# Optimization experiments

Hardware: AMD Instinct MI355X
Metric: run time of the kernel (lower is better)

The kernel has to match this reference:

```python
import jax, jax.numpy as jnp
import numpy as np

D = 256
H = 4
DH = D // H
DFF = 1024
EPS = 1e-5


def _split_heads(x):
    B, L, _ = x.shape
    return x.reshape(B, L, H, DH).transpose(0, 2, 1, 3)  # [B,H,L,dh]


def _merge_heads(o):
    B, h, L, dh = o.shape
    return o.transpose(0, 2, 1, 3).reshape(B, L, h * dh)


def _attention(Q, K, V, M):
    # Q,K,V: [B,H,Lq/Lk,dh]; M: [B,Lq,Lk] or [B,1,Lk]
    A = jnp.einsum('bhqd,bhkd->bhqk', Q, K) / (DH ** 0.5)
    A = jnp.where(M[:, None] == 0, -jnp.inf, A)
    A = jax.nn.softmax(A, axis=-1)
    return jnp.einsum('bhqk,bhkd->bhqd', A, V)


def _layernorm(x, g, b):
    mu = jnp.mean(x, axis=-1, keepdims=True)
    var = jnp.mean(jnp.square(x - mu), axis=-1, keepdims=True)
    return (x - mu) * jax.lax.rsqrt(var + EPS) * g + b


def setup_inputs() -> dict:
    key = jax.random.key(0)
    ks = jax.random.split(key, 14)
    B, T, S = 16, 1024, 1024
    s = 1.0 / (D ** 0.5)
    inp = {
        'X_target': jax.random.normal(ks[0], (B, T, D), jnp.float32),
        'outputMask': jnp.ones((B, T), jnp.float32),
        'X_encoder': jax.random.normal(ks[1], (B, S, D), jnp.float32),
        'inputMask': jnp.ones((B, S), jnp.float32),
        'Wq1': jax.random.normal(ks[2], (D, D), jnp.float32) * s,
        'Wk1': jax.random.normal(ks[3], (D, D), jnp.float32) * s,
        'Wv1': jax.random.normal(ks[4], (D, D), jnp.float32) * s,
        'Wo1': jax.random.normal(ks[5], (D, D), jnp.float32) * s,
        'Wq2': jax.random.normal(ks[6], (D, D), jnp.float32) * s,
        'Wk2': jax.random.normal(ks[7], (D, D), jnp.float32) * s,
        'Wv2': jax.random.normal(ks[8], (D, D), jnp.float32) * s,
        'Wo2': jax.random.normal(ks[9], (D, D), jnp.float32) * s,
        'W1': jax.random.normal(ks[10], (DFF, D), jnp.float32) * s,
        'W2': jax.random.normal(ks[11], (D, DFF), jnp.float32) * (1.0 / (DFF ** 0.5)),
        'g1': jnp.ones((D,), jnp.float32), 'b1': jnp.zeros((D,), jnp.float32),
        'g2': jnp.ones((D,), jnp.float32), 'b2': jnp.zeros((D,), jnp.float32),
        'g3': jnp.ones((D,), jnp.float32), 'b3': jnp.zeros((D,), jnp.float32),
    }
    return inp


def reference(X_target, outputMask, X_encoder, inputMask,
              Wq1, Wk1, Wv1, Wo1, Wq2, Wk2, Wv2, Wo2,
              W1, W2, g1, b1, g2, b2, g3, b3):
    T = X_target.shape[1]
    # combined causal * padding mask (intended tril of ones)
    tril = jnp.tril(jnp.ones((T, T), X_target.dtype))
    M_self = outputMask[:, None, :] * tril  # [B,T,T]
    M_cross = inputMask[:, None, :]         # [B,1,S]

    # masked self-attention (Linear: x @ W.T)
    Q = _split_heads(X_target @ Wq1.T)
    K = _split_heads(X_target @ Wk1.T)
    V = _split_heads(X_target @ Wv1.T)
    O = _merge_heads(_attention(Q, K, V, M_self)) @ Wo1.T
    X = X_target + _layernorm(O, g1, b1)  # AddNorm (dropout eval=identity)

    # cross-attention; note: output proj is O @ Wo2 (no transpose) in source
    Q = _split_heads(X @ Wq2.T)
    K = _split_heads(X_encoder @ Wk2.T)
    V = _split_heads(X_encoder @ Wv2.T)
    O = _merge_heads(_attention(Q, K, V, M_cross)) @ Wo2
    X = X + _layernorm(O, g2, b2)

    # FFN with ReLU after both linears (as in source)
    F = jax.nn.relu(jax.nn.relu(X @ W1.T) @ W2.T)
    X = X + _layernorm(F, g3, b3)
    return X
```

## Files before the change

### kernel.cpp

```cpp
#include <hip/hip_runtime.h>
#include <math.h>

#define D_ 256
#define H_ 4
#define DH_ 64
#define NKT_ 16
#define TPB_BITS 10
#define SCL2E_ 0.18033688011112042f

typedef __attribute__((ext_vector_type(8))) short bf16x8;
typedef __attribute__((ext_vector_type(4))) short short4v;
typedef __attribute__((ext_vector_type(4))) float f32x4;

__device__ __forceinline__ short f2bf(float x) {
  union { float f; unsigned u; } c; c.f = x;
  unsigned r = (c.u + 0x7fffu + ((c.u >> 16) & 1u)) >> 16;
  return (short)r;
}
__device__ __forceinline__ float bf2f(short s) {
  union { unsigned u; float f; } c; c.u = ((unsigned)(unsigned short)s) << 16;
  return c.f;
}
__device__ __forceinline__ unsigned cvtpk(float lo, float hi) {
  unsigned r;
  asm("v_cvt_pk_bf16_f32 %0, %1, %2" : "=v"(r) : "v"(lo), "v"(hi));
  return r;
}
#if __has_builtin(__builtin_amdgcn_exp2f)
#define EXP2F(x) __builtin_amdgcn_exp2f(x)
#else
#define EXP2F(x) __expf(0.6931471805599453f * (x))
#endif

__device__ __forceinline__ void gl_lds16(const void* g, void* lds) {
  __builtin_amdgcn_global_load_lds((const __attribute__((address_space(1))) void*)g,
                                   (__attribute__((address_space(3))) void*)lds,
                                   16, 0, 0);
}

__global__ __launch_bounds__(256) void mask_bias(const float* __restrict__ m0,
                                                 const float* __restrict__ m1,
                                                 float* __restrict__ o0,
                                                 float* __restrict__ o1,
                                                 float* __restrict__ f0,
                                                 float* __restrict__ f1, int n) {
  int i = blockIdx.x * 256 + threadIdx.x;
  if (i < n) {
    o0[i] = (m0[i] != 0.f) ? 0.f : -1e30f;
    o1[i] = (m1[i] != 0.f) ? 0.f : -1e30f;
  }
  if (blockIdx.x == 0) {
    int t = threadIdx.x;
    const float* ms = m0 + (t >> 4) * 1024 + (t & 15) * 64;
    const float* mc = m1 + (t >> 4) * 1024 + (t & 15) * 64;
    float fs = 0.f, fc = 0.f;
    for (int j = 0; j < 64; ++j) {
      if (ms[j] == 0.f) fs = 1.f;
      if (mc[j] == 0.f) fc = 1.f;
    }
    f0[t] = fs; f1[t] = fc;
  }
}

template<int BN, int BK, bool ABF16, bool TRANSB, bool RELU, bool CBF16>
__global__ __launch_bounds__(256) void gemm_mfma(
    const void* __restrict__ A0, const void* __restrict__ A1, const void* __restrict__ A2,
    const float* __restrict__ B0, const float* __restrict__ B1, const float* __restrict__ B2,
    void* __restrict__ C0, void* __restrict__ C1, void* __restrict__ C2,
    int N, int K, int M, int vtrans_z, int ktile_z, int abf16_z, int qscale_z) {
  constexpr int STR = BK + 8;
  __shared__ short Al[2][128][STR];
  __shared__ short Bl[2][BN][STR];
  const int tid = threadIdx.x;
  const int w   = tid >> 6;
  const int l   = tid & 63;
  const int bn  = blockIdx.x * 128;
  const int bm  = blockIdx.y * BN;
  const int z   = blockIdx.z;
  const void*  Av = (z == 0) ? A0 : ((z == 1) ? A1 : A2);
  const float* B  = (z == 0) ? B0 : ((z == 1) ? B1 : B2);
  void*        Cv = (z == 0) ? C0 : ((z == 1) ? C1 : C2);
  const bool abf = ABF16 || (z == abf16_z);
  constexpr int NI = BN / 32;
  const int wm = (w >> 1) * 64;
  const int wn = (w & 1) * (BN / 2);
  const int fr = l & 15;
  const int fg = l >> 4;

  f32x4 acc[4][NI];
  #pragma unroll
  for (int mi = 0; mi < 4; ++mi)
    #pragma unroll
    for (int ni = 0; ni < NI; ++ni) acc[mi][ni] = (f32x4){0.f, 0.f, 0.f, 0.f};

  const int sr = tid >> 1;
  const int sc = (tid & 1) * (BK / 2);
  constexpr int ARF = BK / 8;
  constexpr int ARB = BK / 16;
  constexpr int BRF = (BN == 128) ? (BK / 8) : (BK / 16);
  const int brT = (BN == 128) ? (tid >> 1) : (tid >> 2);
  const int bcT = (BN == 128) ? ((tid & 1) * (BK / 2)) : ((tid & 3) * (BK / 4));

  float4 arf[ARF]; bf16x8 arb[ARB]; float4 brf[BRF > ARF ? BRF : ARF];

  auto loadA = [&](int k0) {
    if (abf) {
      const short* arow = (const short*)Av + (size_t)(bn + sr) * K + k0 + sc;
      #pragma unroll
      for (int i = 0; i < ARB; ++i) arb[i] = *(const bf16x8*)&arow[i * 8];
    } else {
      const float* arow = (const float*)Av + (size_t)(bn + sr) * K + k0 + sc;
      #pragma unroll
      for (int i = 0; i < ARF; ++i) arf[i] = *(const float4*)&arow[i * 4];
    }
  };
  auto loadB = [&](int k0) {
    if (TRANSB) {
      const float* brow = B + (size_t)(bm + brT) * K + k0 + bcT;
      #pragma unroll
      for (int i = 0; i < BRF; ++i) brf[i] = *(const float4*)&brow[i * 4];
    } else {
      #pragma unroll
      for (int i = 0; i < BRF; ++i) {
        int idx = tid + i * 256;
        int kk = (BN == 128) ? (idx >> 5) : (idx >> 4);
        int c4 = (BN == 128) ? ((idx & 31) * 4) : ((idx & 15) * 4);
        brf[i] = *(const float4*)&B[(size_t)(k0 + kk) * M + bm + c4];
      }
    }
  };
  auto store = [&](int buf) {
    if (abf) {
      #pragma unroll
      for (int i = 0; i < ARB; ++i) *(bf16x8*)&Al[buf][sr][sc + i * 8] = arb[i];
    } else {
      #pragma unroll
      for (int i = 0; i < ARF; ++i) {
        float4 v = arf[i];
        short4v s; s[0] = f2bf(v.x); s[1] = f2bf(v.y); s[2] = f2bf(v.z); s[3] = f2bf(v.w);
        *(short4v*)&Al[buf][sr][sc + i * 4] = s;
      }
    }
    if (TRANSB) {
      #pragma unroll
      for (int i = 0; i < BRF; ++i) {
        float4 v = brf[i];
        short4v s; s[0] = f2bf(v.x); s[1] = f2bf(v.y); s[2] = f2bf(v.z); s[3] = f2bf(v.w);
        *(short4v*)&Bl[buf][brT][bcT + i * 4] = s;
      }
    } else {
      #pragma unroll
      for (int i = 0; i < BRF; ++i) {
        int idx = tid + i * 256;
        int kk = (BN == 128) ? (idx >> 5) : (idx >> 4);
        int c4 = (BN == 128) ? ((idx & 31) * 4) : ((idx & 15) * 4);
        float4 v = brf[i];
        Bl[buf][c4 + 0][kk] = f2bf(v.x);
        Bl[buf][c4 + 1][kk] = f2bf(v.y);
        Bl[buf][c4 + 2][kk] = f2bf(v.z);
        Bl[buf][c4 + 3][kk] = f2bf(v.w);
      }
    }
  };

  loadA(0); loadB(0); store(0);
  __syncthreads();
  const int nk = K / BK;
  for (int s = 0; s < nk; ++s) {
    const int cur = s & 1;
    if (s + 1 < nk) { loadA((s + 1) * BK); loadB((s + 1) * BK); }
    #pragma unroll
    for (int kh = 0; kh < BK / 32; ++kh) {
      bf16x8 af[4], bfr[NI];
      #pragma unroll
      for (int mi = 0; mi < 4; ++mi)
        af[mi] = *(bf16x8*)&Al[cur][wm + mi * 16 + fr][kh * 32 + fg * 8];
      #pragma unroll
      for (int ni = 0; ni < NI; ++ni)
        bfr[ni] = *(bf16x8*)&Bl[cur][wn + ni * 16 + fr][kh * 32 + fg * 8];
      #pragma unroll
      for (int mi = 0; mi < 4; ++mi)
        #pragma unroll
        for (int ni = 0; ni < NI; ++ni)
          acc[mi][ni] = __builtin_amdgcn_mfma_f32_16x16x32_bf16(af[mi], bfr[ni], acc[mi][ni], 0, 0, 0);
    }
    if (s + 1 < nk) store(cur ^ 1);
    __syncthreads();
  }

  bool done = false;
  if constexpr (BN == 128) {
    if (z == vtrans_z) {
      done = true;
      #pragma unroll
      for (int mi = 0; mi < 4; ++mi) {
        int nbase = bn + wm + mi * 16 + fg * 4;
        int b_  = nbase >> TPB_BITS;
        int key = nbase & ((1 << TPB_BITS) - 1);
        int kt  = key >> 6, kin = key & 63;
        #pragma unroll
        for (int ni = 0; ni < 4; ++ni) {
          int col = bm + wn + ni * 16 + fr;
          int h_ = col >> 6, dh = col & 63;
          uint2 u;
          u.x = cvtpk(acc[mi][ni][0], acc[mi][ni][1]);
          u.y = cvtpk(acc[mi][ni][2], acc[mi][ni][3]);
          size_t off = ((((size_t)(b_ * H_ + h_) * NKT_) + kt) << 12)
                     + dh * 64 + (((kin >> 3) ^ (dh & 7)) << 3) + (kin & 7);
          *(uint2*)&((short*)Cv)[off] = u;
        }
      }
    } else if (z == ktile_z) {
      done = true;
      #pragma unroll
      for (int mi = 0; mi < 4; ++mi) {
        #pragma unroll
        for (int reg = 0; reg < 4; ++reg) {
          int tok = bn + wm + mi * 16 + fg * 4 + reg;
          int b_  = tok >> TPB_BITS;
          int key = tok & ((1 << TPB_BITS) - 1);
          int kt  = key >> 6, kin = key & 63;
          int fk  = (kin & 3) | (((kin >> 3) & 1) << 2);
          size_t tb = ((((size_t)(b_ * H_) * NKT_) + kt) << 12) + kin * 64;
          #pragma unroll
          for (int ni = 0; ni < 4; ++ni) {
            int col = bm + wn + ni * 16 + fr;
            int h_ = col >> 6, dh = col & 63;
            size_t off = tb + (((size_t)h_ * NKT_) << 12)
                       + (((dh >> 3) ^ fk) << 3) + (dh & 7);
            ((short*)Cv)[off] = f2bf(acc[mi][ni][reg]);
          }
        }
      }
    }
  }
  if (!done) {
    const float cs = (z == qscale_z) ? SCL2E_ : 1.f;
    #pragma unroll
    for (int mi = 0; mi < 4; ++mi) {
      #pragma unroll
      for (int reg = 0; reg < 4; ++reg) {
        size_t rowbase = (size_t)(bn + wm + mi * 16 + fg * 4 + reg) * M + bm + wn;
        #pragma unroll
        for (int ni = 0; ni < NI; ++ni) {
          float v = acc[mi][ni][reg] * cs;
          if (RELU) v = fmaxf(v, 0.f);
          if (CBF16) ((short*)Cv)[rowbase + ni * 16 + fr] = f2bf(v);
          else       ((float*)Cv)[rowbase + ni * 16 + fr] = v;
        }
      }
    }
  }
}

template<bool CAUSAL>
__global__ __launch_bounds__(256) void attn_mfma(const short* __restrict__ Q,
                                                 const short* __restrict__ KT,
                                                 const short* __restrict__ VT,
                                                 const float* __restrict__ bias,
                                                 const float* __restrict__ flags,
                                                 short* __restrict__ O,
                                                 int T, int Lk) {
  __shared__ short Kl[2][64][64];
  __shared__ short Vl[2][64][64];
  const int tid = threadIdx.x;
  const int l   = tid & 63;
  const int w   = tid >> 6;
  const int bh  = blockIdx.x;
  const int b   = bh >> 2;
  const int h   = bh & 3;
  const int r   = l & 15;
  const int g   = l >> 4;

  const short* Ktile = KT + (((size_t)bh * (Lk >> 6)) << 12);
  const short* Vtile = VT + (((size_t)bh * (Lk >> 6)) << 12);
  const float* brow  = bias + (size_t)b * Lk;
  const float* bfl   = flags + b * NKT_;

  const int qt  = CAUSAL ? ((T >> 6) - 1 - (int)blockIdx.y) : (int)blockIdx.y;
  const int nkt = CAUSAL ? (qt + 1) : (Lk >> 6);

  bf16x8 qf[2];
  {
    const short* qrow = Q + ((size_t)(b * T + qt * 64 + w * 16 + r)) * D_ + h * DH_;
    qf[0] = *(const bf16x8*)&qrow[g * 8];
    qf[1] = *(const bf16x8*)&qrow[32 + g * 8];
  }

  float m = -1e30f, ls = 0.f;
  f32x4 acc[4];
  #pragma unroll
  for (int dt = 0; dt < 4; ++dt) acc[dt] = (f32x4){0.f, 0.f, 0.f, 0.f};

  auto stage = [&](int kt, int bb) {
    const short* ks = Ktile + ((size_t)kt << 12) + w * 1024 + (size_t)l * 8;
    const short* vs = Vtile + ((size_t)kt << 12) + w * 1024 + (size_t)l * 8;
    char* kd = (char*)&Kl[bb][0][0] + w * 2048;
    char* vd = (char*)&Vl[bb][0][0] + w * 2048;
    gl_lds16(ks,       kd);
    gl_lds16(ks + 512, kd + 1024);
    gl_lds16(vs,       vd);
    gl_lds16(vs + 512, vd + 1024);
  };

  stage(0, 0);
  __syncthreads();

  const int rx = r & 7;
  const int rowp = 8 * (r >> 2) + (r & 3);
  for (int kt = 0; kt < nkt; ++kt) {
    const int buf = kt & 1;
    if (kt + 1 < nkt) stage(kt + 1, buf ^ 1);

    const char* kb = (const char*)&Kl[buf][0][0];
    const char* vb = (const char*)&Vl[buf][0][0];

    f32x4 sfr[4];
    #pragma unroll
    for (int st = 0; st < 4; ++st) sfr[st] = (f32x4){0.f, 0.f, 0.f, 0.f};
    __builtin_amdgcn_s_setprio(1);
    #pragma unroll
    for (int st = 0; st < 4; ++st) {
      const int rowk = 32 * (st >> 1) + 4 * (st & 1) + rowp;
      #pragma unroll
      for (int kh = 0; kh < 2; ++kh) {
        bf16x8 kf = *(const bf16x8*)(kb + rowk * 128 + (((kh * 4 + g) ^ rx) << 4));
        sfr[st] = __builtin_amdgcn_mfma_f32_16x16x32_bf16(kf, qf[kh], sfr[st], 0, 0, 0);
      }
    }
    __builtin_amdgcn_s_setprio(0);

    float sc[4][4];
    if (bfl[kt] != 0.f) {
      #pragma unroll
      for (int st = 0; st < 4; ++st) {
        float4 mv = *(const float4*)&brow[kt * 64 + 32 * (st >> 1) + 4 * (st & 1) + 8 * g];
        sc[st][0] = sfr[st][0] + mv.x;
        sc[st][1] = sfr[st][1] + mv.y;
        sc[st][2] = sfr[st][2] + mv.z;
        sc[st][3] = sfr[st][3] + mv.w;
      }
    } else {
      #pragma unroll
      for (int st = 0; st < 4; ++st)
        #pragma unroll
        for (int reg = 0; reg < 4; ++reg) sc[st][reg] = sfr[st][reg];
    }
    if (CAUSAL && kt == qt) {
      #pragma unroll
      for (int st = 0; st < 4; ++st)
        #pragma unroll
        for (int reg = 0; reg < 4; ++reg)
          if (32 * (st >> 1) + 4 * (st & 1) + 8 * g + reg > w * 16 + r)
            sc[st][reg] = -1e30f;
    }

    float t0 = fmaxf(fmaxf(sc[0][0], sc[0][1]), sc[0][2]);
    float t1 = fmaxf(fmaxf(sc[0][3], sc[1][0]), sc[1][1]);
    float t2 = fmaxf(fmaxf(sc[1][2], sc[1][3]), sc[2][0]);
    float t3 = fmaxf(fmaxf(sc[2][1], sc[2][2]), sc[2][3]);
    float t4 = fmaxf(fmaxf(sc[3][0], sc[3][1]), sc[3][2]);
    float tm = fmaxf(fmaxf(fmaxf(t0, t1), fmaxf(t2, t3)), fmaxf(t4, sc[3][3]));
    tm = fmaxf(tm, __shfl_xor(tm, 16));
    tm = fmaxf(tm, __shfl_xor(tm, 32));
    const int need = __any(tm - m > 8.f);
    float mnew = need ? fmaxf(m, tm) : m;
    float pe[4][4];
    #pragma unroll
    for (int st = 0; st < 4; ++st)
      #pragma unroll
      for (int reg = 0; reg < 4; ++reg)
        pe[st][reg] = EXP2F(sc[st][reg] - mnew);
    float ps0 = (pe[0][0] + pe[0][1]) + (pe[0][2] + pe[0][3]);
    float ps1 = (pe[1][0] + pe[1][1]) + (pe[1][2] + pe[1][3]);
    float ps2 = (pe[2][0] + pe[2][1]) + (pe[2][2] + pe[2][3]);
    float ps3 = (pe[3][0] + pe[3][1]) + (pe[3][2] + pe[3][3]);
    float psum = (ps0 + ps1) + (ps2 + ps3);
    psum += __shfl_xor(psum, 16);
    psum += __shfl_xor(psum, 32);

    union { unsigned u[4]; bf16x8 v; } pa, pb;
    pa.u[0] = cvtpk(pe[0][0], pe[0][1]);
    pa.u[1] = cvtpk(pe[0][2], pe[0][3]);
    pa.u[2] = cvtpk(pe[1][0], pe[1][1]);
    pa.u[3] = cvtpk(pe[1][2], pe[1][3]);
    pb.u[0] = cvtpk(pe[2][0], pe[2][1]);
    pb.u[1] = cvtpk(pe[2][2], pe[2][3]);
    pb.u[2] = cvtpk(pe[3][0], pe[3][1]);
    pb.u[3] = cvtpk(pe[3][2], pe[3][3]);

    if (need) {
      float alpha = EXP2F(m - mnew);
      ls = ls * alpha + psum;
      m = mnew;
      float af[4];
      #pragma unroll
      for (int reg = 0; reg < 4; ++reg) af[reg] = __shfl(alpha, g * 4 + reg);
      #pragma unroll
      for (int dt = 0; dt < 4; ++dt)
        #pragma unroll
        for (int reg = 0; reg < 4; ++reg) acc[dt][reg] *= af[reg];
    } else {
      ls += psum;
    }

    __builtin_amdgcn_s_setprio(1);
    #pragma unroll
    for (int kh = 0; kh < 2; ++kh) {
      bf16x8 pf = (kh == 0) ? pa.v : pb.v;
      #pragma unroll
      for (int dt = 0; dt < 4; ++dt) {
        bf16x8 vf = *(const bf16x8*)(vb + (dt * 16 + r) * 128 + (((kh * 4 + g) ^ rx) << 4));
        acc[dt] = __builtin_amdgcn_mfma_f32_16x16x32_bf16(pf, vf, acc[dt], 0, 0, 0);
      }
    }
    __builtin_amdgcn_s_setprio(0);

    __syncthreads();
  }

  float inv = (ls > 0.f) ? (1.f / ls) : 0.f;
  float invf[4];
  #pragma unroll
  for (int reg = 0; reg < 4; ++reg) invf[reg] = __shfl(inv, g * 4 + reg);
  #pragma unroll
  for (int reg = 0; reg < 4; ++reg) {
    short* orow = O + ((size_t)(b * T + qt * 64 + w * 16 + g * 4 + reg)) * D_ + h * DH_;
    #pragma unroll
    for (int dt = 0; dt < 4; ++dt)
      orow[dt * 16 + r] = f2bf(acc[dt][reg] * invf[reg]);
  }
}

template<bool RBF16, bool OBF16>
__global__ __launch_bounds__(256) void ln_res(const short* __restrict__ F,
                                              const void* __restrict__ Rv,
                                              const float* __restrict__ g,
                                              const float* __restrict__ bt,
                                              void* __restrict__ outv) {
  const int lane = threadIdx.x & 63;
  const int wid  = threadIdx.x >> 6;
  const size_t row  = (size_t)blockIdx.x * 4 + wid;
  const size_t base = row * 256 + (size_t)lane * 4;
  short4v fv = *(const short4v*)&F[base];
  float vx = bf2f(fv[0]), vy = bf2f(fv[1]), vz = bf2f(fv[2]), vw = bf2f(fv[3]);
  float s = vx + vy + vz + vw;
  #pragma unroll
  for (int o = 32; o >= 1; o >>= 1) s += __shfl_xor(s, o);
  float mu = s * (1.f / 256.f);
  float dx = vx - mu, dy = vy - mu, dz = vz - mu, dw = vw - mu;
  float vr = dx * dx + dy * dy + dz * dz + dw * dw;
  #pragma unroll
  for (int o = 32; o >= 1; o >>= 1) vr += __shfl_xor(vr, o);
  float rstd = rsqrtf(vr * (1.f / 256.f) + 1e-5f);
  float4 g4 = *(const float4*)&g[lane * 4];
  float4 b4 = *(const float4*)&bt[lane * 4];
  float rx, ry, rz, rw;
  if (RBF16) {
    short4v r4 = *(const short4v*)&((const short*)Rv)[base];
    rx = bf2f(r4[0]); ry = bf2f(r4[1]); rz = bf2f(r4[2]); rw = bf2f(r4[3]);
  } else {
    float4 r4 = *(const float4*)&((const float*)Rv)[base];
    rx = r4.x; ry = r4.y; rz = r4.z; rw = r4.w;
  }
  float ox = fmaf(dx * rstd, g4.x, b4.x) + rx;
  float oy = fmaf(dy * rstd, g4.y, b4.y) + ry;
  float oz = fmaf(dz * rstd, g4.z, b4.z) + rz;
  float ow = fmaf(dw * rstd, g4.w, b4.w) + rw;
  if (OBF16) {
    uint2 u; u.x = cvtpk(ox, oy); u.y = cvtpk(oz, ow);
    *(uint2*)&((short*)outv)[base] = u;
  } else {
    *(float4*)&((float*)outv)[base] = make_float4(ox, oy, oz, ow);
  }
}

extern "C" void kernel_launch(void* const* d_in, const int* in_sizes, int n_in,
                              void* d_out, int out_size, void* d_ws, size_t ws_size,
                              hipStream_t stream) {
  const float* Xt    = (const float*)d_in[0];
  const float* oMask = (const float*)d_in[1];
  const float* Xe    = (const float*)d_in[2];
  const float* iMask = (const float*)d_in[3];
  const float* Wq1   = (const float*)d_in[4];
  const float* Wk1   = (const float*)d_in[5];
  const float* Wv1   = (const float*)d_in[6];
  const float* Wo1   = (const float*)d_in[7];
  const float* Wq2   = (const float*)d_in[8];
  const float* Wk2   = (const float*)d_in[9];
  const float* Wv2   = (const float*)d_in[10];
  const float* Wo2   = (const float*)d_in[11];
  const float* W1    = (const float*)d_in[12];
  const float* W2    = (const float*)d_in[13];
  const float* g1    = (const float*)d_in[14];
  const float* b1    = (const float*)d_in[15];
  const float* g2    = (const float*)d_in[16];
  const float* b2    = (const float*)d_in[17];
  const float* g3    = (const float*)d_in[18];
  const float* b3    = (const float*)d_in[19];

  const int B = 16, T = 1024, S = 1024;
  const int NT = B * T;
  const size_t SZ = (size_t)NT * 256;

  float* ws = (float*)d_ws;
  float* s0 = ws;
  float* s1 = ws + SZ;
  float* s2 = ws + 2 * SZ;
  float* s3 = ws + 3 * SZ;
  float* s4 = ws + 4 * SZ;
  float* s5 = ws + 5 * SZ;
  short* b_s0 = (short*)s0; short* b_s1 = (short*)s1; short* b_s2 = (short*)s2;
  short* b_s3 = (short*)s3; short* b_s4 = (short*)s4; short* b_s5 = (short*)s5;
  float* biasS = s3 + 3 * (SZ / 4);
  float* biasC = biasS + B * S;
  float* flagS = biasC + B * S;
  float* flagC = flagS + B * NKT_;

  dim3 blk(256);
  dim3 gQKV(NT / 128, 2, 3);
  dim3 gS64(NT / 128, 4, 1);
  dim3 gF1(NT / 128, 8, 1);
  dim3 gA(B * H_, T / 64);

  mask_bias<<<64, blk, 0, stream>>>(oMask, iMask, biasS, biasC, flagS, flagC, B * T);

  gemm_mfma<128, 32, false, true, false, true><<<gQKV, blk, 0, stream>>>(
      Xt, Xt, Xt, Wq1, Wk1, Wv1, s0, s1, s2, NT, 256, 256, 2, 1, -1, 0);
  attn_mfma<true><<<gA, blk, 0, stream>>>(b_s0, b_s1, b_s2, biasS, flagS, b_s3, T, T);
  gemm_mfma<64, 64, true, true, false, true><<<gS64, blk, 0, stream>>>(
      s3, s3, s3, Wo1, Wo1, Wo1, s0, s0, s0, NT, 256, 256, -1, -1, -1, -1);
  ln_res<false, true><<<NT / 4, blk, 0, stream>>>(b_s0, Xt, g1, b1, b_s4);

  gemm_mfma<128, 32, false, true, false, true><<<gQKV, blk, 0, stream>>>(
      s4, Xe, Xe, Wq2, Wk2, Wv2, s0, s1, s2, NT, 256, 256, 2, 1, 0, 0);
  attn_mfma<false><<<gA, blk, 0, stream>>>(b_s0, b_s1, b_s2, biasC, flagC, b_s3, T, S);
  gemm_mfma<64, 64, true, false, false, true><<<gS64, blk, 0, stream>>>(
      s3, s3, s3, Wo2, Wo2, Wo2, s0, s0, s0, NT, 256, 256, -1, -1, -1, -1);
  ln_res<true, true><<<NT / 4, blk, 0, stream>>>(b_s0, b_s4, g2, b2, b_s5);

  gemm_mfma<128, 32, true, true, true, true><<<gF1, blk, 0, stream>>>(
      s5, s5, s5, W1, W1, W1, s0, s0, s0, NT, 256, 1024, -1, -1, -1, -1);
  gemm_mfma<64, 64, true, true, true, true><<<gS64, blk, 0, stream>>>(
      s0, s0, s0, W2, W2, W2, s4, s4, s4, NT, 1024, 256, -1, -1, -1, -1);
  ln_res<true, false><<<NT / 4, blk, 0, stream>>>(b_s4, b_s5, g3, b3, (float*)d_out);
}
```

Measured before the change: 197.7 us.

## Split attention over key range into two partial passes with a merge kernel

Splits each attention query tile's key loop into two halves, the first eight key tiles and the rest, each run by a separate block along a new grid z dimension. Each block writes an unnormalized partial output and its running max and sum. A new merge kernel then combines the two halves into the normalized output. This adds parallelism and balances causal work across blocks, at the cost of an extra kernel launch, extra global traffic for the partials, bf16 rounding of unnormalized partials, and dropping LDS double-buffering in favour of a single synchronized buffer.

```diff
diff --git a/kernel.cpp b/kernel.cpp
--- a/kernel.cpp
+++ b/kernel.cpp
@@ -5,6 +5,7 @@
 #define H_ 4
 #define DH_ 64
 #define NKT_ 16
+#define NT_ 16384
 #define TPB_BITS 10
 #define SCL2E_ 0.18033688011112042f
 
@@ -259,16 +260,18 @@
                                                  const short* __restrict__ VT,
                                                  const float* __restrict__ bias,
                                                  const float* __restrict__ flags,
-                                                 short* __restrict__ O,
+                                                 short* __restrict__ Pp,
+                                                 float2* __restrict__ st,
                                                  int T, int Lk) {
-  __shared__ short Kl[2][64][64];
-  __shared__ short Vl[2][64][64];
+  __shared__ short Kl[64][64];
+  __shared__ short Vl[64][64];
   const int tid = threadIdx.x;
   const int l   = tid & 63;
   const int w   = tid >> 6;
   const int bh  = blockIdx.x;
   const int b   = bh >> 2;
   const int h   = bh & 3;
+  const int z   = blockIdx.z;
   const int r   = l & 15;
   const int g   = l >> 4;
 
@@ -277,8 +280,18 @@
   const float* brow  = bias + (size_t)b * Lk;
   const float* bfl   = flags + b * NKT_;
 
-  const int qt  = CAUSAL ? ((T >> 6) - 1 - (int)blockIdx.y) : (int)blockIdx.y;
-  const int nkt = CAUSAL ? (qt + 1) : (Lk >> 6);
+  const int qt   = CAUSAL ? ((T >> 6) - 1 - (int)blockIdx.y) : (int)blockIdx.y;
+  const int full = CAUSAL ? (qt + 1) : (Lk >> 6);
+  const int kt0  = z ? 8 : 0;
+  const int kt1  = z ? full : (full < 8 ? full : 8);
+
+  float m = -1e30f, ls = 0.f;
+
+  if (kt1 <= kt0) {
+    if (l < 16)
+      st[((size_t)z * 64 + bh) * 1024 + qt * 64 + w * 16 + l] = make_float2(m, ls);
+    return;
+  }
 
   bf16x8 qf[2];
   {
@@ -287,45 +300,42 @@
     qf[1] = *(const bf16x8*)&qrow[32 + g * 8];
   }
 
-  float m = -1e30f, ls = 0.f;
   f32x4 acc[4];
   #pragma unroll
   for (int dt = 0; dt < 4; ++dt) acc[dt] = (f32x4){0.f, 0.f, 0.f, 0.f};
 
-  auto stage = [&](int kt, int bb) {
+  auto stage = [&](int kt) {
     const short* ks = Ktile + ((size_t)kt << 12) + w * 1024 + (size_t)l * 8;
     const short* vs = Vtile + ((size_t)kt << 12) + w * 1024 + (size_t)l * 8;
-    char* kd = (char*)&Kl[bb][0][0] + w * 2048;
-    char* vd = (char*)&Vl[bb][0][0] + w * 2048;
+    char* kd = (char*)&Kl[0][0] + w * 2048;
+    char* vd = (char*)&Vl[0][0] + w * 2048;
     gl_lds16(ks,       kd);
     gl_lds16(ks + 512, kd + 1024);
     gl_lds16(vs,       vd);
     gl_lds16(vs + 512, vd + 1024);
   };
 
-  stage(0, 0);
-  __syncthreads();
-
   const int rx = r & 7;
   const int rowp = 8 * (r >> 2) + (r & 3);
-  for (int kt = 0; kt < nkt; ++kt) {
-    const int buf = kt & 1;
-    if (kt + 1 < nkt) stage(kt + 1, buf ^ 1);
-
-    const char* kb = (const char*)&Kl[buf][0][0];
-    const char* vb = (const char*)&Vl[buf][0][0];
+  const char* kb = (const char*)&Kl[0][0];
+  const char* vb = (const char*)&Vl[0][0];
+
+  for (int kt = kt0; kt < kt1; ++kt) {
+    if (kt > kt0) __syncthreads();
+    stage(kt);
+    __syncthreads();
 
     f32x4 sfr[4];
     #pragma unroll
-    for (int st = 0; st < 4; ++st) sfr[st] = (f32x4){0.f, 0.f, 0.f, 0.f};
+    for (int stt = 0; stt < 4; ++stt) sfr[stt] = (f32x4){0.f, 0.f, 0.f, 0.f};
     __builtin_amdgcn_s_setprio(1);
     #pragma unroll
-    for (int st = 0; st < 4; ++st) {
-      const int rowk = 32 * (st >> 1) + 4 * (st & 1) + rowp;
+    for (int stt = 0; stt < 4; ++stt) {
+      const int rowk = 32 * (stt >> 1) + 4 * (stt & 1) + rowp;
       #pragma unroll
       for (int kh = 0; kh < 2; ++kh) {
         bf16x8 kf = *(const bf16x8*)(kb + rowk * 128 + (((kh * 4 + g) ^ rx) << 4));
-        sfr[st] = __builtin_amdgcn_mfma_f32_16x16x32_bf16(kf, qf[kh], sfr[st], 0, 0, 0);
+        sfr[stt] = __builtin_amdgcn_mfma_f32_16x16x32_bf16(kf, qf[kh], sfr[stt], 0, 0, 0);
       }
     }
     __builtin_amdgcn_s_setprio(0);
@@ -333,26 +343,26 @@
     float sc[4][4];
     if (bfl[kt] != 0.f) {
       #pragma unroll
-      for (int st = 0; st < 4; ++st) {
-        float4 mv = *(const float4*)&brow[kt * 64 + 32 * (st >> 1) + 4 * (st & 1) + 8 * g];
-        sc[st][0] = sfr[st][0] + mv.x;
-        sc[st][1] = sfr[st][1] + mv.y;
-        sc[st][2] = sfr[st][2] + mv.z;
-        sc[st][3] = sfr[st][3] + mv.w;
+      for (int stt = 0; stt < 4; ++stt) {
+        float4 mv = *(const float4*)&brow[kt * 64 + 32 * (stt >> 1) + 4 * (stt & 1) + 8 * g];
+        sc[stt][0] = sfr[stt][0] + mv.x;
+        sc[stt][1] = sfr[stt][1] + mv.y;
+        sc[stt][2] = sfr[stt][2] + mv.z;
+        sc[stt][3] = sfr[stt][3] + mv.w;
       }
     } else {
       #pragma unroll
-      for (int st = 0; st < 4; ++st)
-        #pragma unroll
-        for (int reg = 0; reg < 4; ++reg) sc[st][reg] = sfr[st][reg];
+      for (int stt = 0; stt < 4; ++stt)
+        #pragma unroll
+        for (int reg = 0; reg < 4; ++reg) sc[stt][reg] = sfr[stt][reg];
     }
     if (CAUSAL && kt == qt) {
       #pragma unroll
-      for (int st = 0; st < 4; ++st)
+      for (int stt = 0; stt < 4; ++stt)
         #pragma unroll
         for (int reg = 0; reg < 4; ++reg)
-          if (32 * (st >> 1) + 4 * (st & 1) + 8 * g + reg > w * 16 + r)
-            sc[st][reg] = -1e30f;
+          if (32 * (stt >> 1) + 4 * (stt & 1) + 8 * g + reg > w * 16 + r)
+            sc[stt][reg] = -1e30f;
     }
 
     float t0 = fmaxf(fmaxf(sc[0][0], sc[0][1]), sc[0][2]);
@@ -367,10 +377,10 @@
     float mnew = need ? fmaxf(m, tm) : m;
     float pe[4][4];
     #pragma unroll
-    for (int st = 0; st < 4; ++st)
+    for (int stt = 0; stt < 4; ++stt)
       #pragma unroll
       for (int reg = 0; reg < 4; ++reg)
-        pe[st][reg] = EXP2F(sc[st][reg] - mnew);
+        pe[stt][reg] = EXP2F(sc[stt][reg] - mnew);
     float ps0 = (pe[0][0] + pe[0][1]) + (pe[0][2] + pe[0][3]);
     float ps1 = (pe[1][0] + pe[1][1]) + (pe[1][2] + pe[1][3]);
     float ps2 = (pe[2][0] + pe[2][1]) + (pe[2][2] + pe[2][3]);
@@ -415,21 +425,46 @@
       }
     }
     __builtin_amdgcn_s_setprio(0);
-
-    __syncthreads();
-  }
-
-  float inv = (ls > 0.f) ? (1.f / ls) : 0.f;
-  float invf[4];
-  #pragma unroll
-  for (int reg = 0; reg < 4; ++reg) invf[reg] = __shfl(inv, g * 4 + reg);
+  }
+
+  short* pbase = Pp + (size_t)z * ((size_t)NT_ * 256);
   #pragma unroll
   for (int reg = 0; reg < 4; ++reg) {
-    short* orow = O + ((size_t)(b * T + qt * 64 + w * 16 + g * 4 + reg)) * D_ + h * DH_;
+    short* prow = pbase + ((size_t)(b * T + qt * 64 + w * 16 + g * 4 + reg)) * D_ + h * DH_;
     #pragma unroll
     for (int dt = 0; dt < 4; ++dt)
-      orow[dt * 16 + r] = f2bf(acc[dt][reg] * invf[reg]);
-  }
+      prow[dt * 16 + r] = f2bf(acc[dt][reg]);
+  }
+  if (l < 16)
+    st[((size_t)z * 64 + bh) * 1024 + qt * 64 + w * 16 + l] = make_float2(m, ls);
+}
+
+__global__ __launch_bounds__(256) void attn_merge(const short* __restrict__ P,
+                                                  const float2* __restrict__ st,
+                                                  short* __restrict__ O) {
+  const int lane = threadIdx.x & 63;
+  const int wid  = threadIdx.x >> 6;
+  const int row  = blockIdx.x * 4 + wid;
+  const int b    = row >> TPB_BITS;
+  const int q    = row & ((1 << TPB_BITS) - 1);
+  const int h    = lane >> 4;
+  const int bh   = b * H_ + h;
+  float2 s0 = st[(size_t)bh * 1024 + q];
+  float2 s1 = st[(size_t)(64 + bh) * 1024 + q];
+  float mm = fmaxf(s0.x, s1.x);
+  float a0 = EXP2F(s0.x - mm), a1 = EXP2F(s1.x - mm);
+  float den = a0 * s0.y + a1 * s1.y;
+  float inv = (den > 0.f) ? (1.f / den) : 0.f;
+  a0 *= inv; a1 *= inv;
+  size_t base = (size_t)row * 256 + (size_t)lane * 4;
+  short4v p0 = *(const short4v*)&P[base];
+  short4v p1 = *(const short4v*)&P[(size_t)NT_ * 256 + base];
+  uint2 u;
+  u.x = cvtpk(a0 * bf2f(p0[0]) + a1 * bf2f(p1[0]),
+              a0 * bf2f(p0[1]) + a1 * bf2f(p1[1]));
+  u.y = cvtpk(a0 * bf2f(p0[2]) + a1 * bf2f(p1[2]),
+              a0 * bf2f(p0[3]) + a1 * bf2f(p1[3]));
+  *(uint2*)&O[base] = u;
 }
 
 template<bool RBF16, bool OBF16>
@@ -510,38 +545,44 @@
   float* s3 = ws + 3 * SZ;
   float* s4 = ws + 4 * SZ;
   float* s5 = ws + 5 * SZ;
-  short* b_s0 = (short*)s0; short* b_s1 = (short*)s1; short* b_s2 = (short*)s2;
-  short* b_s3 = (short*)s3; short* b_s4 = (short*)s4; short* b_s5 = (short*)s5;
+  short* b_s0 = (short*)s0; short* b_s3 = (short*)s3;
+  short* b_s4 = (short*)s4; short* b_s5 = (short*)s5;
   float* biasS = s3 + 3 * (SZ / 4);
   float* biasC = biasS + B * S;
   float* flagS = biasC + B * S;
   float* flagC = flagS + B * NKT_;
+  float2* stat = (float2*)(flagC + B * NKT_);
 
   dim3 blk(256);
   dim3 gQKV(NT / 128, 2, 3);
   dim3 gS64(NT / 128, 4, 1);
   dim3 gF1(NT / 128, 8, 1);
-  dim3 gA(B * H_, T / 64);
+  dim3 gA(B * H_, T / 64, 2);
+  dim3 gM(NT / 4);
 
   mask_bias<<<64, blk, 0, stream>>>(oMask, iMask, biasS, biasC, flagS, flagC, B * T);
 
   gemm_mfma<128, 32, false, true, false, true><<<gQKV, blk, 0, stream>>>(
       Xt, Xt, Xt, Wq1, Wk1, Wv1, s0, s1, s2, NT, 256, 256, 2, 1, -1, 0);
-  attn_mfma<true><<<gA, blk, 0, stream>>>(b_s0, b_s1, b_s2, biasS, flagS, b_s3, T, T);
+  attn_mfma<true><<<gA, blk, 0, stream>>>((const short*)s0, (const short*)s1, (const short*)s2,
+                                          biasS, flagS, b_s5, stat, T, T);
+  attn_merge<<<gM, blk, 0, stream>>>(b_s5, stat, b_s3);
   gemm_mfma<64, 64, true, true, false, true><<<gS64, blk, 0, stream>>>(
       s3, s3, s3, Wo1, Wo1, Wo1, s0, s0, s0, NT, 256, 256, -1, -1, -1, -1);
-  ln_res<false, true><<<NT / 4, blk, 0, stream>>>(b_s0, Xt, g1, b1, b_s4);
+  ln_res<false, true><<<gM, blk, 0, stream>>>(b_s0, Xt, g1, b1, b_s4);
 
   gemm_mfma<128, 32, false, true, false, true><<<gQKV, blk, 0, stream>>>(
       s4, Xe, Xe, Wq2, Wk2, Wv2, s0, s1, s2, NT, 256, 256, 2, 1, 0, 0);
-  attn_mfma<false><<<gA, blk, 0, stream>>>(b_s0, b_s1, b_s2, biasC, flagC, b_s3, T, S);
+  attn_mfma<false><<<gA, blk, 0, stream>>>((const short*)s0, (const short*)s1, (const short*)s2,
+                                           biasC, flagC, b_s5, stat, T, S);
+  attn_merge<<<gM, blk, 0, stream>>>(b_s5, stat, b_s3);
   gemm_mfma<64, 64, true, false, false, true><<<gS64, blk, 0, stream>>>(
       s3, s3, s3, Wo2, Wo2, Wo2, s0, s0, s0, NT, 256, 256, -1, -1, -1, -1);
-  ln_res<true, true><<<NT / 4, blk, 0, stream>>>(b_s0, b_s4, g2, b2, b_s5);
+  ln_res<true, true><<<gM, blk, 0, stream>>>(b_s0, b_s4, g2, b2, b_s5);
 
   gemm_mfma<128, 32, true, true, true, true><<<gF1, blk, 0, stream>>>(
       s5, s5, s5, W1, W1, W1, s0, s0, s0, NT, 256, 1024, -1, -1, -1, -1);
   gemm_mfma<64, 64, true, true, true, true><<<gS64, blk, 0, stream>>>(
       s0, s0, s0, W2, W2, W2, s4, s4, s4, NT, 1024, 256, -1, -1, -1, -1);
-  ln_res<true, false><<<NT / 4, blk, 0, stream>>>(b_s4, b_s5, g3, b3, (float*)d_out);
-}
+  ln_res<true, false><<<gM, blk, 0, stream>>>(b_s4, b_s5, g3, b3, (float*)d_out);
+}
```

Measured after the change: 208.3 us. 5.3% more time.
